# Performance work log

Hardware: AMD Instinct MI355X
Metric: run time of the kernel (lower is better)

Reference implementation:

```python
import jax, jax.numpy as jnp
import numpy as np
from jax.scipy.linalg import solve_triangular

B, L, HID, NH = 2, 1024, 1024, 4
DK = DV = 256
CONV_K, CHUNK, FIR_S_K, FIR_L_K = 4, 32, 3, 31
GATE_IN = HID + 3 * DV * 4 + DV * 4  # 5120
GATE_H = 2 * DV  # 512


def _l2norm(x):
    return x * jax.lax.rsqrt(jnp.sum(x * x, -1, keepdims=True) + 1e-6)


def _short_conv(x, w):
    # causal depthwise conv1d + silu. x: [b,l,c], w: [c,k]
    c, k = w.shape
    y = jax.lax.conv_general_dilated(x.transpose(0, 2, 1), w[:, None, :], (1,),
                                     [(k - 1, 0)], feature_group_count=c)
    return jax.nn.silu(y.transpose(0, 2, 1))


def _fir(x, f):
    # per-head depthwise causal FIR. x: [b,l,h,d], f: [h,d,k]
    b, l, h, d = x.shape
    k = f.shape[-1]
    xf = x.transpose(0, 2, 3, 1).reshape(b, h * d, l)
    y = jax.lax.conv_general_dilated(xf, f.reshape(h * d, 1, k), (1,),
                                     [(k - 1, 0)], feature_group_count=h * d)
    return y.reshape(b, h, d, l).transpose(0, 3, 1, 2)


def _delta_rule(q, k, v, beta, chunk=CHUNK):
    # q,k: [b,h,L,dk], v: [b,h,L,dv], beta: [b,h,L]; L % chunk == 0
    b, h, l, dk = q.shape
    dv = v.shape[-1]
    n = l // chunk
    q = _l2norm(q)
    k = _l2norm(k)
    v = v * beta[..., None]
    kb = k * beta[..., None]
    rs = lambda t: t.reshape(b, h, n, chunk, -1)
    q, k, v, kb = map(rs, (q, k, v, kb))
    # UT transform: serial forward substitution == unit-lower triangular solve
    A = -jnp.tril(jnp.einsum('bhncd,bhned->bhnce', kb, k), -1)  # strictly lower
    eye = jnp.eye(chunk, dtype=q.dtype)
    T = solve_triangular(eye - A, jnp.broadcast_to(eye, A.shape), lower=True)
    u = T @ v   # [b,h,n,c,dv]
    w = T @ kb  # [b,h,n,c,dk]
    mov = lambda t: jnp.moveaxis(t, 2, 0)

    def step(S, inp):
        qi, ki, ui, wi = inp  # [b,h,c,d]
        attn = jnp.tril(qi @ ki.transpose(0, 1, 3, 2))  # causal incl. diag
        u_i = ui - wi @ S
        o_i = qi @ S + attn @ u_i
        return S + ki.transpose(0, 1, 3, 2) @ u_i, o_i

    S0 = jnp.zeros((b, h, dk, dv), dtype=q.dtype)
    S, o = jax.lax.scan(step, S0, (mov(q), mov(k), mov(u), mov(w)))
    o = jnp.moveaxis(o, 0, 2).reshape(b, h, l, dv)
    return o, S


def _gate(hidden, branches, W1, b1, W2, b2, temp, eps_floor):
    def stats(p):
        m = p.mean(-1, keepdims=True)
        r = jnp.sqrt(jnp.clip((p * p).mean(-1, keepdims=True), 1e-8))
        mx = p.max(-1, keepdims=True)
        return jnp.concatenate([jnp.broadcast_to(m, p.shape),
                                jnp.broadcast_to(r, p.shape),
                                jnp.broadcast_to(mx, p.shape)], -1)

    b, l, h, d = branches[0].shape
    hb = jnp.broadcast_to(hidden[:, :, None, :], (b, l, h, hidden.shape[-1]))
    head_in = jnp.concatenate([hb] + [stats(p) for p in branches] + list(branches), -1)
    hmid = jax.nn.gelu(head_in @ W1 + b1, approximate=False)
    logits = hmid @ W2 + b2  # [b,l,h,4]
    t = jnp.clip(temp, 0.2, 10.0)[None, None, :, None]
    w = jax.nn.softmax(logits / t, -1)
    floor = jnp.clip(eps_floor, 1e-7, 0.1)[None, None]
    w = jnp.maximum(w, floor)
    return w / w.sum(-1, keepdims=True)


def setup_inputs() -> dict:
    key = jax.random.key(0)
    ks = jax.random.split(key, 16)
    s = 0.02
    inp = {
        'x': jax.random.normal(ks[0], (B, L, HID), jnp.float32),
        'Wq': jax.random.normal(ks[1], (HID, NH * DK), jnp.float32) * s,
        'Wk': jax.random.normal(ks[2], (HID, NH * DK), jnp.float32) * s,
        'Wv': jax.random.normal(ks[3], (HID, NH * DV), jnp.float32) * s,
        'Wb': jax.random.normal(ks[4], (HID, NH), jnp.float32) * s,
        'qc_w': jax.random.normal(ks[5], (NH * DK, CONV_K), jnp.float32) * 0.5,
        'kc_w': jax.random.normal(ks[6], (NH * DK, CONV_K), jnp.float32) * 0.5,
        'vc_w': jax.random.normal(ks[7], (NH * DV, CONV_K), jnp.float32) * 0.5,
        'gW1': jax.random.normal(ks[10], (GATE_IN, GATE_H), jnp.float32) * s,
        'gb1': jnp.zeros((GATE_H,), jnp.float32),
        'gW2': jax.random.normal(ks[11], (GATE_H, 4), jnp.float32) * s,
        'gb2': jnp.zeros((4,), jnp.float32),
        'temp': jnp.ones((NH,), jnp.float32),
        'eps_floor': jnp.full((NH, 4), 0.01, jnp.float32),
        'onorm_w': jnp.ones((DV,), jnp.float32),
        'Wo': jax.random.normal(ks[12], (NH * DV, HID), jnp.float32) * s,
    }
    # FIR filters: identity tap at last position + small noise (matches init intent)
    fs = jnp.zeros((NH, DV, FIR_S_K)).at[..., -1].set(1.0)
    fl = jnp.zeros((NH, DV, FIR_L_K)).at[..., -1].set(1.0)
    inp['fir_s'] = fs + s * jax.random.normal(ks[8], fs.shape, jnp.float32)
    inp['fir_l'] = fl + s * jax.random.normal(ks[9], fl.shape, jnp.float32)
    return inp


def reference(x, Wq, Wk, Wv, Wb, qc_w, kc_w, vc_w, fir_s, fir_l,
              gW1, gb1, gW2, gb2, temp, eps_floor, onorm_w, Wo):
    b, l, _ = x.shape
    q = _short_conv(x @ Wq, qc_w).reshape(b, l, NH, DK)
    k = _short_conv(x @ Wk, kc_w).reshape(b, l, NH, DK)
    v = _short_conv(x @ Wv, vc_w).reshape(b, l, NH, DV)
    beta = jax.nn.sigmoid(x @ Wb)  # [b,l,h]
    tr = lambda t: t.transpose(0, 2, 1, 3)
    delta_o, _ = _delta_rule(tr(q), tr(k), tr(v), beta.transpose(0, 2, 1))
    delta_o = tr(delta_o)  # [b,l,h,dv]
    branches = [_fir(v, fir_s), _fir(v, fir_l), delta_o, v]
    w = _gate(x, branches, gW1, gb1, gW2, gb2, temp, eps_floor)
    o = sum(w[..., i:i + 1] * branches[i] for i in range(4))
    o = o * jax.lax.rsqrt((o * o).mean(-1, keepdims=True) + 1e-5) * onorm_w
    return o.reshape(b, l, NH * DV) @ Wo
```

## Files before the change

kernel.cpp:

```cpp
#include <hip/hip_runtime.h>
#include <math.h>

#define BB 2
#define LL 1024
#define HIDD 1024
#define NH 4
#define DD 256
#define NCH 32
#define ROWS 2048
#define HROWS 8192

typedef long long i64;
typedef unsigned short u16t;
typedef unsigned int u32t;
typedef __attribute__((ext_vector_type(8))) short short8;
typedef __attribute__((ext_vector_type(4))) float f32x4;
#define MFMA_BF16(a, b, c) __builtin_amdgcn_mfma_f32_16x16x32_bf16(a, b, c, 0, 0, 0)

__device__ __forceinline__ float sigmoidf_(float x) { return 1.0f / (1.0f + expf(-x)); }

__device__ __forceinline__ u16t f2bf(float f) {
  u32t u = __float_as_uint(f);
  u = u + 0x7FFFu + ((u >> 16) & 1u);
  return (u16t)(u >> 16);
}
__device__ __forceinline__ u32t pk2(u16t a, u16t b) { return (u32t)a | ((u32t)b << 16); }

__device__ __forceinline__ u32t cvt_pk_bf16(float lo, float hi) {
  u32t r;
  asm("v_cvt_pk_bf16_f32 %0, %1, %2" : "=v"(r) : "v"(lo), "v"(hi));
  return r;
}

__device__ __forceinline__ void async_load16(const u16t* g, u16t* l) {
  __builtin_amdgcn_global_load_lds(
      (const __attribute__((address_space(1))) u32t*)g,
      (__attribute__((address_space(3))) u32t*)l, 16, 0, 0);
}

__device__ __forceinline__ void barrier_lds_only() {
  asm volatile("s_waitcnt lgkmcnt(0)" ::: "memory");
  __builtin_amdgcn_s_barrier();
  asm volatile("" ::: "memory");
}

template<int N>
__device__ __forceinline__ void block_reduce_sum(float* v, float* scratch) {
  int lane = threadIdx.x & 63, wid = threadIdx.x >> 6;
#pragma unroll
  for (int i = 0; i < N; i++) {
    float x = v[i];
#pragma unroll
    for (int off = 1; off < 64; off <<= 1) x += __shfl_xor(x, off);
    if (lane == 0) scratch[wid * N + i] = x;
  }
  __syncthreads();
#pragma unroll
  for (int i = 0; i < N; i++)
    v[i] = scratch[i] + scratch[N + i] + scratch[2 * N + i] + scratch[3 * N + i];
  __syncthreads();
}

__device__ __forceinline__ void transcast_body(
    const float* __restrict__ in, int ldin, u16t* __restrict__ out, int ldout,
    int nbi, int kbi, float (*tile)[33]) {
  int tx = threadIdx.x & 31, ty = threadIdx.x >> 5;
  int nb = nbi * 32, kb = kbi * 32;
#pragma unroll
  for (int r = 0; r < 4; r++)
    tile[ty + r * 8][tx] = in[(i64)(kb + ty + r * 8) * ldin + nb + tx];
  __syncthreads();
#pragma unroll
  for (int r = 0; r < 4; r++)
    out[(i64)(nb + ty + r * 8) * ldout + kb + tx] = f2bf(tile[tx][ty + r * 8]);
}

__global__ __launch_bounds__(256) void prep_kernel(
    const float* __restrict__ Wq, const float* __restrict__ Wk, const float* __restrict__ Wv,
    const float* __restrict__ x, const float* __restrict__ Wb,
    u16t* __restrict__ WqkvT, u16t* __restrict__ xbf, float* __restrict__ betab) {
  __shared__ float tile[32][33];
  int blk = blockIdx.x, t = threadIdx.x;
  if (blk < 3072) {
    int m = blk >> 10, bi = blk & 1023;
    const float* in = m == 0 ? Wq : m == 1 ? Wk : Wv;
    transcast_body(in, 1024, WqkvT + (i64)m * 1024 * 1024, 1024, bi & 31, bi >> 5, tile);
  } else if (blk < 5120) {
    i64 e = ((i64)(blk - 3072) * 256 + t) * 4;
    float4 v = *(const float4*)(x + e);
    uint2 o;
    o.x = pk2(f2bf(v.x), f2bf(v.y));
    o.y = pk2(f2bf(v.z), f2bf(v.w));
    *(uint2*)(xbf + e) = o;
  } else {
    int row = blk - 5120;
    float a[4] = {0, 0, 0, 0};
    for (int c = t; c < 1024; c += 256) {
      float xv = x[(i64)row * 1024 + c];
      float4 wv = *(const float4*)(Wb + c * 4);
      a[0] += xv * wv.x; a[1] += xv * wv.y; a[2] += xv * wv.z; a[3] += xv * wv.w;
    }
    block_reduce_sum<4>(a, (float*)tile);
    if (t == 0) {
#pragma unroll
      for (int g = 0; g < 4; g++) betab[row * 4 + g] = sigmoidf_(a[g]);
    }
  }
}

__device__ __forceinline__ void gemm_bt_body(
    const u16t* __restrict__ A, const u16t* __restrict__ B,
    float* __restrict__ C, int K, int ldc, int n0, int m0,
    u16t* As, u16t* Bs) {
  int t = threadIdx.x;
  int w = t >> 6, lane = t & 63;
  int l15 = lane & 15, quad = lane >> 4;
  int wm = (w & 1) * 64, wn = (w >> 1) * 64;
  f32x4 acc[4][4] = {};
  int c0 = 2 * w, c1 = 2 * w + 1;
  int srow0 = c0 * 16 + (lane >> 2);
  int srow1 = c1 * 16 + (lane >> 2);
  int scol = (lane & 3) * 8;
  const u16t* Ag0 = A + (i64)(m0 + srow0) * K + scol;
  const u16t* Ag1 = A + (i64)(m0 + srow1) * K + scol;
  const u16t* Bg0 = B + (i64)(n0 + srow0) * K + scol;
  const u16t* Bg1 = B + (i64)(n0 + srow1) * K + scol;
  int lb0 = c0 * 512, lb1 = c1 * 512;
  async_load16(Ag0, As + lb0);
  async_load16(Ag1, As + lb1);
  async_load16(Bg0, Bs + lb0);
  async_load16(Bg1, Bs + lb1);
  __syncthreads();
  int nt = K >> 5;
  for (int ti = 0; ti < nt; ++ti) {
    int cur = (ti & 1) << 12;
    if (ti + 1 < nt) {
      int nxt = ((ti + 1) & 1) << 12;
      int k = (ti + 1) << 5;
      async_load16(Ag0 + k, As + nxt + lb0);
      async_load16(Ag1 + k, As + nxt + lb1);
      async_load16(Bg0 + k, Bs + nxt + lb0);
      async_load16(Bg1 + k, Bs + nxt + lb1);
    }
    short8 a[4], b[4];
#pragma unroll
    for (int mt = 0; mt < 4; mt++)
      a[mt] = *(const short8*)&As[cur + (wm + mt * 16 + l15) * 32 + quad * 8];
#pragma unroll
    for (int ntt = 0; ntt < 4; ntt++)
      b[ntt] = *(const short8*)&Bs[cur + (wn + ntt * 16 + l15) * 32 + quad * 8];
#pragma unroll
    for (int mt = 0; mt < 4; mt++)
#pragma unroll
      for (int ntt = 0; ntt < 4; ntt++)
        acc[mt][ntt] = MFMA_BF16(a[mt], b[ntt], acc[mt][ntt]);
    __syncthreads();
  }
#pragma unroll
  for (int mt = 0; mt < 4; mt++) {
    int r0 = m0 + wm + mt * 16 + quad * 4;
#pragma unroll
    for (int nt2 = 0; nt2 < 4; nt2++) {
      int cc = n0 + wn + nt2 * 16 + l15;
#pragma unroll
      for (int rg = 0; rg < 4; rg++)
        C[(i64)(r0 + rg) * ldc + cc] = acc[mt][nt2][rg];
    }
  }
}

__global__ __launch_bounds__(256) void gemm_bt_kernel(
    const u16t* __restrict__ A, const u16t* __restrict__ B,
    float* __restrict__ C, int K, int ldc) {
  __shared__ u16t As[2 * 128 * 32];
  __shared__ u16t Bs[2 * 128 * 32];
  gemm_bt_body(A, B, C, K, ldc, blockIdx.x * 128, blockIdx.y * 128, As, Bs);
}

__global__ __launch_bounds__(256) void conv_silu3_kernel(
    const float* __restrict__ pre, const float* __restrict__ qw,
    const float* __restrict__ kw, const float* __restrict__ vw,
    float* __restrict__ qo, float* __restrict__ ko, float* __restrict__ vo,
    u16t* __restrict__ brcat) {
  int seg = blockIdx.x >> 11;
  int row = blockIdx.x & 2047;
  int l = row & 1023;
  int c = threadIdx.x * 4;
  const float* w = seg == 0 ? qw : seg == 1 ? kw : vw;
  float* out = seg == 0 ? qo : seg == 1 ? ko : vo;
  float4 w0 = *(const float4*)(w + (i64)(c + 0) * 4);
  float4 w1 = *(const float4*)(w + (i64)(c + 1) * 4);
  float4 w2 = *(const float4*)(w + (i64)(c + 2) * 4);
  float4 w3 = *(const float4*)(w + (i64)(c + 3) * 4);
  const float* base = pre + (i64)row * 3072 + (seg << 10) + c;
  float4 x0 = *(const float4*)(base);
  float4 acc;
  acc.x = w0.w * x0.x; acc.y = w1.w * x0.y; acc.z = w2.w * x0.z; acc.w = w3.w * x0.w;
  if (l >= 1) {
    float4 xm = *(const float4*)(base - 3072);
    acc.x += w0.z * xm.x; acc.y += w1.z * xm.y; acc.z += w2.z * xm.z; acc.w += w3.z * xm.w;
  }
  if (l >= 2) {
    float4 xm = *(const float4*)(base - 2 * 3072);
    acc.x += w0.y * xm.x; acc.y += w1.y * xm.y; acc.z += w2.y * xm.z; acc.w += w3.y * xm.w;
  }
  if (l >= 3) {
    float4 xm = *(const float4*)(base - 3 * 3072);
    acc.x += w0.x * xm.x; acc.y += w1.x * xm.y; acc.z += w2.x * xm.z; acc.w += w3.x * xm.w;
  }
  float4 r;
  r.x = acc.x * sigmoidf_(acc.x);
  r.y = acc.y * sigmoidf_(acc.y);
  r.z = acc.z * sigmoidf_(acc.z);
  r.w = acc.w * sigmoidf_(acc.w);
  *(float4*)(out + (i64)row * 1024 + c) = r;
  if (seg == 2) {
    uint2 o;
    o.x = cvt_pk_bf16(r.x, r.y);
    o.y = cvt_pk_bf16(r.z, r.w);
    *(uint2*)(brcat + ((i64)row * 4 + (c >> 8)) * 1024 + 768 + (c & 255)) = o;
  }
}

__global__ __launch_bounds__(256) void preprocess_kernel(
    const float* __restrict__ q, const float* __restrict__ k, const float* __restrict__ v,
    const float* __restrict__ beta, float* __restrict__ qn, float* __restrict__ kn,
    float* __restrict__ vb, float* __restrict__ kb, u16t* __restrict__ qnbf) {
  int t = threadIdx.x, lane = t & 63, wv = t >> 6;
  int row = blockIdx.x * 4 + wv;
  i64 base = (i64)row * 256 + lane * 4;
  float4 q4 = *(const float4*)(q + base);
  float4 k4 = *(const float4*)(k + base);
  float4 v4 = *(const float4*)(v + base);
  float s2[2];
  s2[0] = q4.x * q4.x + q4.y * q4.y + q4.z * q4.z + q4.w * q4.w;
  s2[1] = k4.x * k4.x + k4.y * k4.y + k4.z * k4.z + k4.w * k4.w;
#pragma unroll
  for (int off = 1; off < 64; off <<= 1) {
    s2[0] += __shfl_xor(s2[0], off);
    s2[1] += __shfl_xor(s2[1], off);
  }
  float qi = rsqrtf(s2[0] + 1e-6f), ki = rsqrtf(s2[1] + 1e-6f);
  float bet = beta[row];
  float4 qn4, kn4, vb4, kb4;
  qn4.x = q4.x * qi; qn4.y = q4.y * qi; qn4.z = q4.z * qi; qn4.w = q4.w * qi;
  kn4.x = k4.x * ki; kn4.y = k4.y * ki; kn4.z = k4.z * ki; kn4.w = k4.w * ki;
  vb4.x = v4.x * bet; vb4.y = v4.y * bet; vb4.z = v4.z * bet; vb4.w = v4.w * bet;
  kb4.x = kn4.x * bet; kb4.y = kn4.y * bet; kb4.z = kn4.z * bet; kb4.w = kn4.w * bet;
  *(float4*)(qn + base) = qn4;
  *(float4*)(kn + base) = kn4;
  *(float4*)(vb + base) = vb4;
  *(float4*)(kb + base) = kb4;
  int b = row >> 12, l = (row >> 2) & 1023, h = row & 3;
  uint2 o;
  o.x = cvt_pk_bf16(qn4.x, qn4.y);
  o.y = cvt_pk_bf16(qn4.z, qn4.w);
  *(uint2*)(qnbf + ((i64)(b * 4 + h) * 1024 + l) * 256 + lane * 4) = o;
}

__global__ __launch_bounds__(256) void phaseA2_kernel(
    const float* __restrict__ qn, const float* __restrict__ kn,
    const float* __restrict__ vb, const float* __restrict__ kb,
    float* __restrict__ u_g, u16t* __restrict__ w_bf, u16t* __restrict__ attn_bf,
    u16t* __restrict__ knT,
    const float* __restrict__ gW1, const float* __restrict__ Wo,
    u16t* __restrict__ W1hT, u16t* __restrict__ W1bT, u16t* __restrict__ WoT,
    float* __restrict__ wsum) {
  __shared__ __attribute__((aligned(16))) char smem[37376];
  int blk = blockIdx.x, t = threadIdx.x;
  if (blk < 256) {
    float (*KN)[260] = (float(*)[260])smem;
    float (*Ms)[32] = (float(*)[32])(smem + 33280);
    int i = blk & 31, bh = blk >> 5;
    int rbase = ((bh >> 2) * LL + i * 32) * NH + (bh & 3);
    i64 bhn = blk;
#pragma unroll
    for (int ii = 0; ii < 8; ii++) {
      int fid = t + ii * 256;
      int c = fid >> 6, dq = (fid & 63) << 2;
      *(float4*)&KN[c][dq] = *(const float4*)(kn + (i64)(rbase + c * NH) * 256 + dq);
    }
    __syncthreads();
    int c = t >> 3, e0 = (t & 7) * 4;
    const float* kbp = kb + (i64)(rbase + c * NH) * 256;
    const float* qp = qn + (i64)(rbase + c * NH) * 256;
    float am[4] = {0, 0, 0, 0}, aa[4] = {0, 0, 0, 0};
    for (int d = 0; d < 256; d += 4) {
      float4 kv = *(const float4*)(kbp + d);
      float4 qv = *(const float4*)(qp + d);
#pragma unroll
      for (int z = 0; z < 4; z++) {
        float4 nv = *(const float4*)&KN[e0 + z][d];
        am[z] += kv.x * nv.x + kv.y * nv.y + kv.z * nv.z + kv.w * nv.w;
        aa[z] += qv.x * nv.x + qv.y * nv.y + qv.z * nv.z + qv.w * nv.w;
      }
    }
    {
      uint2 o;
      u16t a0 = (e0 + 0 <= c) ? f2bf(aa[0]) : 0;
      u16t a1 = (e0 + 1 <= c) ? f2bf(aa[1]) : 0;
      u16t a2 = (e0 + 2 <= c) ? f2bf(aa[2]) : 0;
      u16t a3 = (e0 + 3 <= c) ? f2bf(aa[3]) : 0;
      o.x = pk2(a0, a1); o.y = pk2(a2, a3);
      *(uint2*)(attn_bf + bhn * 1024 + c * 32 + e0) = o;
    }
#pragma unroll
    for (int z = 0; z < 4; z++) {
      int e = e0 + z;
      Ms[c][e] = (e < c) ? am[z] : 0.0f;
    }
    __syncthreads();
    float uc[32], wc[32];
#pragma unroll
    for (int cc = 0; cc < 32; cc++) {
      float uval = vb[(i64)(rbase + cc * NH) * 256 + t];
      float wval = kb[(i64)(rbase + cc * NH) * 256 + t];
#pragma unroll
      for (int c2 = 0; c2 < cc; c2++) {
        float m = Ms[cc][c2];
        uval -= m * uc[c2];
        wval -= m * wc[c2];
      }
      uc[cc] = uval; wc[cc] = wval;
      u_g[(bhn * 32 + cc) * 256 + t] = uval;
      w_bf[(bhn * 32 + cc) * 256 + t] = f2bf(-wval);
    }
    int d = t;
    u16t o[32];
#pragma unroll
    for (int cc = 0; cc < 32; cc++) o[cc] = f2bf(KN[cc][d]);
#pragma unroll
    for (int z = 0; z < 4; z++) {
      uint4 vv;
      vv.x = pk2(o[z * 8 + 0], o[z * 8 + 1]);
      vv.y = pk2(o[z * 8 + 2], o[z * 8 + 3]);
      vv.z = pk2(o[z * 8 + 4], o[z * 8 + 5]);
      vv.w = pk2(o[z * 8 + 6], o[z * 8 + 7]);
      *(uint4*)(knT + (bhn * 256 + d) * 32 + z * 8) = vv;
    }
  } else if (blk < 2304) {
    float (*tile)[33] = (float(*)[33])smem;
    int pb = blk - 256;
    if (pb < 1024) {
      int which = pb >> 9, bi = pb & 511;
      const float* in = gW1 + (which ? (i64)4096 * 512 : 0);
      transcast_body(in, 512, which ? W1bT : W1hT, 1024, bi & 15, bi >> 4, tile);
    } else {
      int bi = pb - 1024;
      transcast_body(Wo, 1024, WoT, 1024, bi & 31, bi >> 5, tile);
    }
  } else {
    int bi = blk - 2304;
    int s12 = bi >> 1, col = (bi & 1) * 256 + t;
    const float* p = gW1 + (i64)(1024 + s12 * 256) * 512 + col;
    float acc = 0.0f;
    for (int r = 0; r < 256; r++) acc += p[(i64)r * 512];
    wsum[s12 * 512 + col] = acc;
  }
}

#define SROW 264
struct ScanBuf {
  short8 m8[8];
  f32x4 uc4;
  short8 af;
  short8 kf[4];
};

__device__ void delta_scan_body(
    int blk,
    const u16t* __restrict__ wbf, const u16t* __restrict__ knT,
    const float* __restrict__ u_g, const u16t* __restrict__ qnbf,
    const u16t* __restrict__ attnbf,
    float* __restrict__ dlt, u16t* __restrict__ brcat,
    u16t* Sbf, u16t* Ubf) {
  int t = threadIdx.x, w = t >> 6, lane = t & 63;
  int l15 = lane & 15, quad = lane >> 4;
  int bh = blk & 7, jb = blk >> 3, j0 = jb * 16;
  int b_ = bh >> 2, h_ = bh & 3;
  bool isU = (w < 2);
  int wc = isU ? w : (w - 2);
  for (int idx = t; idx < 16 * SROW; idx += 256) Sbf[idx] = 0;
  f32x4 accS[4] = {};
  __syncthreads();
  __builtin_amdgcn_s_setprio(1);

  auto load_chunk = [&](int i, ScanBuf& B) {
    i64 bhn = (i64)bh * 32 + i;
    const u16t* mbase = isU
        ? wbf + (bhn * 32 + wc * 16 + l15) * 256 + quad * 8
        : qnbf + ((i64)bh * 1024 + i * 32 + wc * 16 + l15) * 256 + quad * 8;
#pragma unroll
    for (int kd = 0; kd < 8; kd++) B.m8[kd] = *(const short8*)(mbase + kd * 32);
    if (isU) {
      int cm = wc * 16 + quad * 4;
#pragma unroll
      for (int r = 0; r < 4; r++)
        B.uc4[r] = u_g[(bhn * 32 + cm + r) * 256 + j0 + l15];
    } else {
      B.af = *(const short8*)(attnbf + bhn * 1024 + (wc * 16 + l15) * 32 + quad * 8);
    }
#pragma unroll
    for (int dt = 0; dt < 4; dt++)
      B.kf[dt] = *(const short8*)(knT + (bhn * 256 + w * 64 + dt * 16 + l15) * 32 + quad * 8);
  };

  auto process = [&](int i, ScanBuf& B) {
    f32x4 zero = {};
    f32x4 ca = isU ? B.uc4 : zero;
    f32x4 cb = zero;
#pragma unroll
    for (int kd = 0; kd < 4; kd++) {
      short8 sfa = *(const short8*)&Sbf[l15 * SROW + kd * 32 + quad * 8];
      short8 sfb = *(const short8*)&Sbf[l15 * SROW + (kd + 4) * 32 + quad * 8];
      ca = MFMA_BF16(B.m8[kd], sfa, ca);
      cb = MFMA_BF16(B.m8[kd + 4], sfb, cb);
    }
    f32x4 cacc;
#pragma unroll
    for (int r = 0; r < 4; r++) cacc[r] = ca[r] + cb[r];
    if (isU) {
      int cm = wc * 16 + quad * 4;
      uint2 o;
      o.x = cvt_pk_bf16(cacc[0], cacc[1]);
      o.y = cvt_pk_bf16(cacc[2], cacc[3]);
      *(uint2*)&Ubf[l15 * 40 + cm] = o;
    }
    barrier_lds_only();
    short8 bu = *(const short8*)&Ubf[l15 * 40 + quad * 8];
    if (!isU) {
      cacc = MFMA_BF16(B.af, bu, cacc);
#pragma unroll
      for (int rg = 0; rg < 4; rg++) {
        int l = i * 32 + wc * 16 + quad * 4 + rg;
        i64 row = ((i64)b_ * 1024 + l) * 4 + h_;
        dlt[row * 256 + j0 + l15] = cacc[rg];
        brcat[row * 1024 + 512 + j0 + l15] = f2bf(cacc[rg]);
      }
    }
#pragma unroll
    for (int dt = 0; dt < 4; dt++) accS[dt] = MFMA_BF16(B.kf[dt], bu, accS[dt]);
#pragma unroll
    for (int dt = 0; dt < 4; dt++) {
      uint2 o;
      o.x = cvt_pk_bf16(accS[dt][0], accS[dt][1]);
      o.y = cvt_pk_bf16(accS[dt][2], accS[dt][3]);
      *(uint2*)&Sbf[l15 * SROW + w * 64 + dt * 16 + quad * 4] = o;
    }
    barrier_lds_only();
  };

  ScanBuf b0, b1;
  load_chunk(0, b0);
#pragma unroll 1
  for (int ii = 0; ii < 16; ii++) {
    int i = ii * 2;
    load_chunk(i + 1, b1);
    process(i, b0);
    if (ii < 15) load_chunk(i + 2, b0);
    process(i + 1, b1);
  }
  __builtin_amdgcn_s_setprio(0);
}

__device__ void fir2_body(
    int blk, const float* __restrict__ v,
    const float* __restrict__ f_s, const float* __restrict__ f_l,
    float* __restrict__ fs, float* __restrict__ fl, u16t* __restrict__ brcat) {
  int t = threadIdx.x;
  int b = blk >> 8, h = (blk >> 6) & 3, lc = blk & 63;
  int l0 = lc * 16;
  float flw[31], fsw[3];
  const float* flp = f_l + ((i64)h * 256 + t) * 31;
#pragma unroll
  for (int j = 0; j < 31; j++) flw[j] = flp[j];
  const float* fsp = f_s + ((i64)h * 256 + t) * 3;
#pragma unroll
  for (int j = 0; j < 3; j++) fsw[j] = fsp[j];
  float win[46];
#pragma unroll
  for (int r = 0; r < 46; r++) {
    int l = l0 - 30 + r;
    win[r] = (l >= 0) ? v[(((i64)b * 1024 + l) * 4 + h) * 256 + t] : 0.0f;
  }
#pragma unroll
  for (int i = 0; i < 16; i++) {
    float al = 0.0f;
#pragma unroll
    for (int j = 0; j < 31; j++) al += flw[j] * win[i + j];
    float as = fsw[0] * win[i + 28] + fsw[1] * win[i + 29] + fsw[2] * win[i + 30];
    i64 row = ((i64)b * 1024 + (l0 + i)) * 4 + h;
    fs[row * 256 + t] = as;
    fl[row * 256 + t] = al;
    brcat[row * 1024 + t] = f2bf(as);
    brcat[row * 1024 + 256 + t] = f2bf(al);
  }
}

__global__ __launch_bounds__(256) void mega5_kernel(
    const u16t* __restrict__ wbf, const u16t* __restrict__ knT,
    const float* __restrict__ u_g, const u16t* __restrict__ qnbf,
    const u16t* __restrict__ attnbf, float* __restrict__ dlt, u16t* __restrict__ brcat,
    const float* __restrict__ vbuf, const float* __restrict__ firs,
    const float* __restrict__ firl, float* __restrict__ fs, float* __restrict__ fl,
    const u16t* __restrict__ xbf, const u16t* __restrict__ W1hT,
    float* __restrict__ hbase) {
  __shared__ __attribute__((aligned(16))) char smem[32768];
  int blk = blockIdx.x;
  if (blk < 128) {
    u16t* Sbf = (u16t*)smem;
    u16t* Ubf = Sbf + 16 * SROW;
    delta_scan_body(blk, wbf, knT, u_g, qnbf, attnbf, dlt, brcat, Sbf, Ubf);
  } else if (blk < 640) {
    fir2_body(blk - 128, vbuf, firs, firl, fs, fl, brcat);
  } else {
    int bi = blk - 640;
    u16t* As = (u16t*)smem;
    u16t* Bs = As + 2 * 128 * 32;
    gemm_bt_body(xbf, W1hT, hbase, 1024, 512, (bi & 3) * 128, (bi >> 2) * 128, As, Bs);
  }
}

__global__ __launch_bounds__(256) void gatemix_kernel(
    const float* __restrict__ hbase, const float* __restrict__ brW,
    const float* __restrict__ wsum,
    const float* __restrict__ gb1, const float* __restrict__ gW2,
    const float* __restrict__ gb2, const float* __restrict__ temp,
    const float* __restrict__ epsf,
    const float* __restrict__ fs, const float* __restrict__ fl,
    const float* __restrict__ dlt, const float* __restrict__ v,
    const float* __restrict__ onw, u16t* __restrict__ out) {
  int t = threadIdx.x, lane = t & 63, wv = t >> 6;
  int row = blockIdx.x * 4 + wv;
  int bl = row >> 2, h = row & 3;
  i64 base = (i64)row * 256 + lane * 4;
  float4 vfs = *(const float4*)(fs + base);
  float4 vfl = *(const float4*)(fl + base);
  float4 vdl = *(const float4*)(dlt + base);
  float4 vvv = *(const float4*)(v + base);
  float r8[8];
  r8[0] = vfs.x + vfs.y + vfs.z + vfs.w;
  r8[1] = vfs.x * vfs.x + vfs.y * vfs.y + vfs.z * vfs.z + vfs.w * vfs.w;
  r8[2] = vfl.x + vfl.y + vfl.z + vfl.w;
  r8[3] = vfl.x * vfl.x + vfl.y * vfl.y + vfl.z * vfl.z + vfl.w * vfl.w;
  r8[4] = vdl.x + vdl.y + vdl.z + vdl.w;
  r8[5] = vdl.x * vdl.x + vdl.y * vdl.y + vdl.z * vdl.z + vdl.w * vdl.w;
  r8[6] = vvv.x + vvv.y + vvv.z + vvv.w;
  r8[7] = vvv.x * vvv.x + vvv.y * vvv.y + vvv.z * vvv.z + vvv.w * vvv.w;
#pragma unroll
  for (int off = 1; off < 64; off <<= 1) {
#pragma unroll
    for (int i = 0; i < 8; i++) r8[i] += __shfl_xor(r8[i], off);
  }
  float m4[4];
  m4[0] = fmaxf(fmaxf(vfs.x, vfs.y), fmaxf(vfs.z, vfs.w));
  m4[1] = fmaxf(fmaxf(vfl.x, vfl.y), fmaxf(vfl.z, vfl.w));
  m4[2] = fmaxf(fmaxf(vdl.x, vdl.y), fmaxf(vdl.z, vdl.w));
  m4[3] = fmaxf(fmaxf(vvv.x, vvv.y), fmaxf(vvv.z, vvv.w));
#pragma unroll
  for (int off = 1; off < 64; off <<= 1) {
#pragma unroll
    for (int i = 0; i < 4; i++) m4[i] = fmaxf(m4[i], __shfl_xor(m4[i], off));
  }
  float st[12];
#pragma unroll
  for (int p = 0; p < 4; p++) {
    st[p * 3 + 0] = r8[p * 2] * (1.0f / 256.0f);
    st[p * 3 + 1] = sqrtf(fmaxf(r8[p * 2 + 1] * (1.0f / 256.0f), 1e-8f));
    st[p * 3 + 2] = m4[p];
  }
  float lg[4] = {0, 0, 0, 0};
#pragma unroll
  for (int jj = 0; jj < 8; jj++) {
    int o = jj * 64 + lane;
    float hm = hbase[(i64)bl * 512 + o] + brW[(i64)row * 512 + o] + gb1[o];
#pragma unroll
    for (int s = 0; s < 12; s++) hm += st[s] * wsum[s * 512 + o];
    float ge = 0.5f * hm * (1.0f + erff(hm * 0.70710678118654752f));
    float4 w2 = *(const float4*)(gW2 + o * 4);
    lg[0] += ge * w2.x; lg[1] += ge * w2.y; lg[2] += ge * w2.z; lg[3] += ge * w2.w;
  }
#pragma unroll
  for (int off = 1; off < 64; off <<= 1) {
#pragma unroll
    for (int i = 0; i < 4; i++) lg[i] += __shfl_xor(lg[i], off);
  }
  float tt = fminf(fmaxf(temp[h], 0.2f), 10.0f);
  float l0 = (lg[0] + gb2[0]) / tt;
  float l1 = (lg[1] + gb2[1]) / tt;
  float l2 = (lg[2] + gb2[2]) / tt;
  float l3 = (lg[3] + gb2[3]) / tt;
  float m = fmaxf(fmaxf(l0, l1), fmaxf(l2, l3));
  float e0 = expf(l0 - m), e1 = expf(l1 - m), e2 = expf(l2 - m), e3 = expf(l3 - m);
  float ssum = e0 + e1 + e2 + e3;
  float w0 = e0 / ssum, w1 = e1 / ssum, w2 = e2 / ssum, w3 = e3 / ssum;
  w0 = fmaxf(w0, fminf(fmaxf(epsf[h * 4 + 0], 1e-7f), 0.1f));
  w1 = fmaxf(w1, fminf(fmaxf(epsf[h * 4 + 1], 1e-7f), 0.1f));
  w2 = fmaxf(w2, fminf(fmaxf(epsf[h * 4 + 2], 1e-7f), 0.1f));
  w3 = fmaxf(w3, fminf(fmaxf(epsf[h * 4 + 3], 1e-7f), 0.1f));
  float s2 = w0 + w1 + w2 + w3;
  float g0 = w0 / s2, g1 = w1 / s2, g2 = w2 / s2, g3 = w3 / s2;
  float4 o4;
  o4.x = g0 * vfs.x + g1 * vfl.x + g2 * vdl.x + g3 * vvv.x;
  o4.y = g0 * vfs.y + g1 * vfl.y + g2 * vdl.y + g3 * vvv.y;
  o4.z = g0 * vfs.z + g1 * vfl.z + g2 * vdl.z + g3 * vvv.z;
  o4.w = g0 * vfs.w + g1 * vfl.w + g2 * vdl.w + g3 * vvv.w;
  float ss = o4.x * o4.x + o4.y * o4.y + o4.z * o4.z + o4.w * o4.w;
#pragma unroll
  for (int off = 1; off < 64; off <<= 1) ss += __shfl_xor(ss, off);
  float scale = rsqrtf(ss * (1.0f / 256.0f) + 1e-5f);
  float4 ow4 = *(const float4*)(onw + lane * 4);
  uint2 ow;
  ow.x = cvt_pk_bf16(o4.x * scale * ow4.x, o4.y * scale * ow4.y);
  ow.y = cvt_pk_bf16(o4.z * scale * ow4.z, o4.w * scale * ow4.w);
  *(uint2*)(out + (i64)bl * 1024 + h * 256 + lane * 4) = ow;
}

extern "C" void kernel_launch(void* const* d_in, const int* in_sizes, int n_in,
                              void* d_out, int out_size, void* d_ws, size_t ws_size,
                              hipStream_t stream) {
  (void)in_sizes; (void)n_in; (void)out_size; (void)ws_size;
  const float* x    = (const float*)d_in[0];
  const float* Wq   = (const float*)d_in[1];
  const float* Wk   = (const float*)d_in[2];
  const float* Wv   = (const float*)d_in[3];
  const float* Wb   = (const float*)d_in[4];
  const float* qcw  = (const float*)d_in[5];
  const float* kcw  = (const float*)d_in[6];
  const float* vcw  = (const float*)d_in[7];
  const float* gW1  = (const float*)d_in[8];
  const float* gb1  = (const float*)d_in[9];
  const float* gW2  = (const float*)d_in[10];
  const float* gb2  = (const float*)d_in[11];
  const float* temp = (const float*)d_in[12];
  const float* epsf = (const float*)d_in[13];
  const float* onw  = (const float*)d_in[14];
  const float* Wo   = (const float*)d_in[15];
  const float* firs = (const float*)d_in[16];
  const float* firl = (const float*)d_in[17];
  float* out = (float*)d_out;

  float* ws = (float*)d_ws;
  float* qkv_pre  = ws + 0;
  float* branchW  = ws + 0;
  float* hbase    = ws + 4194304;
  u16t*  W1hT     = (u16t*)(ws + 5242880);
  u16t*  W1bT     = (u16t*)(ws + 5505024);
  u16t*  WoT      = (u16t*)(ws + 5767168);
  u16t*  brcat    = (u16t*)(ws + 6291456);
  float* qbuf     = ws + 10485760; float* qn = qbuf;
  float* kbuf     = ws + 12582912; float* kn = kbuf;
  float* vbuf     = ws + 14680064;
  float* vb       = ws + 16777216;
  u16t*  omix_bf  = (u16t*)(ws + 16777216);
  float* kb       = ws + 18874368;
  float* dlt      = ws + 18874368;
  float* u_g      = ws + 20971520;
  u16t*  w_bf     = (u16t*)(ws + 23068672);
  u16t*  qn_bf    = (u16t*)(ws + 24117248);
  u16t*  knT      = (u16t*)(ws + 25165824);
  u16t*  attn_bf  = (u16t*)(ws + 26214400);
  float* fs       = ws + 26345472;
  float* fl       = ws + 28442624;
  u16t*  xbf      = (u16t*)(ws + 30539776);
  u16t*  WqkvT    = (u16t*)(ws + 31588352);
  float* betab    = ws + 33161216;
  float* wsum     = ws + 33267712;

  prep_kernel<<<7168, 256, 0, stream>>>(Wq, Wk, Wv, x, Wb, WqkvT, xbf, betab);
  gemm_bt_kernel<<<dim3(24, 16), 256, 0, stream>>>(xbf, WqkvT, qkv_pre, 1024, 3072);
  conv_silu3_kernel<<<6144, 256, 0, stream>>>(qkv_pre, qcw, kcw, vcw, qbuf, kbuf, vbuf, brcat);
  preprocess_kernel<<<2048, 256, 0, stream>>>(qbuf, kbuf, vbuf, betab, qn, kn, vb, kb, qn_bf);
  phaseA2_kernel<<<2328, 256, 0, stream>>>(qn, kn, vb, kb, u_g, w_bf, attn_bf, knT,
                                           gW1, Wo, W1hT, W1bT, WoT, wsum);
  mega5_kernel<<<704, 256, 0, stream>>>(w_bf, knT, u_g, qn_bf, attn_bf, dlt, brcat,
                                        vbuf, firs, firl, fs, fl,
                                        xbf, W1hT, hbase);
  gemm_bt_kernel<<<dim3(4, 64), 256, 0, stream>>>(brcat, W1bT, branchW, 1024, 512);
  gatemix_kernel<<<2048, 256, 0, stream>>>(hbase, branchW, wsum, gb1, gW2, gb2,
                                           temp, epsf, fs, fl, dlt, vbuf, onw, omix_bf);
  gemm_bt_kernel<<<dim3(8, 16), 256, 0, stream>>>(omix_bf, WoT, out, 1024, 1024);
}
```

Before: 316.6 us.

## Move FIR into phaseA kernel and overlap branch GEMM with delta scan

```diff
diff --git a/kernel.cpp b/kernel.cpp
--- a/kernel.cpp
+++ b/kernel.cpp
@@ -108,30 +108,29 @@
   }
 }
 
-__device__ __forceinline__ void gemm_bt_body(
+__device__ __forceinline__ void gemm_tiles_acc(
     const u16t* __restrict__ A, const u16t* __restrict__ B,
-    float* __restrict__ C, int K, int ldc, int n0, int m0,
-    u16t* As, u16t* Bs) {
+    i64 ld, int koff, int Kext, int n0, int m0,
+    u16t* As, u16t* Bs, f32x4 (&acc)[4][4]) {
   int t = threadIdx.x;
   int w = t >> 6, lane = t & 63;
   int l15 = lane & 15, quad = lane >> 4;
   int wm = (w & 1) * 64, wn = (w >> 1) * 64;
-  f32x4 acc[4][4] = {};
   int c0 = 2 * w, c1 = 2 * w + 1;
   int srow0 = c0 * 16 + (lane >> 2);
   int srow1 = c1 * 16 + (lane >> 2);
   int scol = (lane & 3) * 8;
-  const u16t* Ag0 = A + (i64)(m0 + srow0) * K + scol;
-  const u16t* Ag1 = A + (i64)(m0 + srow1) * K + scol;
-  const u16t* Bg0 = B + (i64)(n0 + srow0) * K + scol;
-  const u16t* Bg1 = B + (i64)(n0 + srow1) * K + scol;
+  const u16t* Ag0 = A + (i64)(m0 + srow0) * ld + koff + scol;
+  const u16t* Ag1 = A + (i64)(m0 + srow1) * ld + koff + scol;
+  const u16t* Bg0 = B + (i64)(n0 + srow0) * ld + koff + scol;
+  const u16t* Bg1 = B + (i64)(n0 + srow1) * ld + koff + scol;
   int lb0 = c0 * 512, lb1 = c1 * 512;
   async_load16(Ag0, As + lb0);
   async_load16(Ag1, As + lb1);
   async_load16(Bg0, Bs + lb0);
   async_load16(Bg1, Bs + lb1);
   __syncthreads();
-  int nt = K >> 5;
+  int nt = Kext >> 5;
   for (int ti = 0; ti < nt; ++ti) {
     int cur = (ti & 1) << 12;
     if (ti + 1 < nt) {
@@ -156,17 +155,36 @@
         acc[mt][ntt] = MFMA_BF16(a[mt], b[ntt], acc[mt][ntt]);
     __syncthreads();
   }
+}
+
+__device__ __forceinline__ void gemm_store(
+    float* __restrict__ C, int ldc, int n0, int m0, f32x4 (&acc)[4][4], bool add) {
+  int t = threadIdx.x;
+  int w = t >> 6, lane = t & 63;
+  int l15 = lane & 15, quad = lane >> 4;
+  int wm = (w & 1) * 64, wn = (w >> 1) * 64;
 #pragma unroll
   for (int mt = 0; mt < 4; mt++) {
     int r0 = m0 + wm + mt * 16 + quad * 4;
 #pragma unroll
-    for (int nt2 = 0; nt2 < 4; nt2++) {
-      int cc = n0 + wn + nt2 * 16 + l15;
-#pragma unroll
-      for (int rg = 0; rg < 4; rg++)
-        C[(i64)(r0 + rg) * ldc + cc] = acc[mt][nt2][rg];
-    }
-  }
+    for (int nt = 0; nt < 4; nt++) {
+      int cc = n0 + wn + nt * 16 + l15;
+#pragma unroll
+      for (int rg = 0; rg < 4; rg++) {
+        i64 idx = (i64)(r0 + rg) * ldc + cc;
+        C[idx] = add ? (C[idx] + acc[mt][nt][rg]) : acc[mt][nt][rg];
+      }
+    }
+  }
+}
+
+__device__ __forceinline__ void gemm_bt_body(
+    const u16t* __restrict__ A, const u16t* __restrict__ B,
+    float* __restrict__ C, int K, int ldc, int n0, int m0,
+    u16t* As, u16t* Bs) {
+  f32x4 acc[4][4] = {};
+  gemm_tiles_acc(A, B, K, 0, K, n0, m0, As, Bs, acc);
+  gemm_store(C, ldc, n0, m0, acc, false);
 }
 
 __global__ __launch_bounds__(256) void gemm_bt_kernel(
@@ -258,14 +276,51 @@
   *(uint2*)(qnbf + ((i64)(b * 4 + h) * 1024 + l) * 256 + lane * 4) = o;
 }
 
-__global__ __launch_bounds__(256) void phaseA2_kernel(
+__device__ void fir2_body(
+    int blk, const float* __restrict__ v,
+    const float* __restrict__ f_s, const float* __restrict__ f_l,
+    float* __restrict__ fs, float* __restrict__ fl, u16t* __restrict__ brcat) {
+  int t = threadIdx.x;
+  int b = blk >> 8, h = (blk >> 6) & 3, lc = blk & 63;
+  int l0 = lc * 16;
+  float flw[31], fsw[3];
+  const float* flp = f_l + ((i64)h * 256 + t) * 31;
+#pragma unroll
+  for (int j = 0; j < 31; j++) flw[j] = flp[j];
+  const float* fsp = f_s + ((i64)h * 256 + t) * 3;
+#pragma unroll
+  for (int j = 0; j < 3; j++) fsw[j] = fsp[j];
+  float win[46];
+#pragma unroll
+  for (int r = 0; r < 46; r++) {
+    int l = l0 - 30 + r;
+    win[r] = (l >= 0) ? v[(((i64)b * 1024 + l) * 4 + h) * 256 + t] : 0.0f;
+  }
+#pragma unroll
+  for (int i = 0; i < 16; i++) {
+    float al = 0.0f;
+#pragma unroll
+    for (int j = 0; j < 31; j++) al += flw[j] * win[i + j];
+    float as = fsw[0] * win[i + 28] + fsw[1] * win[i + 29] + fsw[2] * win[i + 30];
+    i64 row = ((i64)b * 1024 + (l0 + i)) * 4 + h;
+    fs[row * 256 + t] = as;
+    fl[row * 256 + t] = al;
+    brcat[row * 1024 + t] = f2bf(as);
+    brcat[row * 1024 + 256 + t] = f2bf(al);
+  }
+}
+
+__global__ __launch_bounds__(256) void phaseA3_kernel(
     const float* __restrict__ qn, const float* __restrict__ kn,
     const float* __restrict__ vb, const float* __restrict__ kb,
     float* __restrict__ u_g, u16t* __restrict__ w_bf, u16t* __restrict__ attn_bf,
     u16t* __restrict__ knT,
     const float* __restrict__ gW1, const float* __restrict__ Wo,
     u16t* __restrict__ W1hT, u16t* __restrict__ W1bT, u16t* __restrict__ WoT,
-    float* __restrict__ wsum) {
+    float* __restrict__ wsum,
+    const float* __restrict__ vbuf, const float* __restrict__ firs,
+    const float* __restrict__ firl, float* __restrict__ fs, float* __restrict__ fl,
+    u16t* __restrict__ brcat) {
   __shared__ __attribute__((aligned(16))) char smem[37376];
   int blk = blockIdx.x, t = threadIdx.x;
   if (blk < 256) {
@@ -349,13 +404,15 @@
       int bi = pb - 1024;
       transcast_body(Wo, 1024, WoT, 1024, bi & 31, bi >> 5, tile);
     }
-  } else {
+  } else if (blk < 2328) {
     int bi = blk - 2304;
     int s12 = bi >> 1, col = (bi & 1) * 256 + t;
     const float* p = gW1 + (i64)(1024 + s12 * 256) * 512 + col;
     float acc = 0.0f;
     for (int r = 0; r < 256; r++) acc += p[(i64)r * 512];
     wsum[s12 * 512 + col] = acc;
+  } else {
+    fir2_body(blk - 2328, vbuf, firs, firl, fs, fl, brcat);
   }
 }
 
@@ -463,62 +520,46 @@
   __builtin_amdgcn_s_setprio(0);
 }
 
-__device__ void fir2_body(
-    int blk, const float* __restrict__ v,
-    const float* __restrict__ f_s, const float* __restrict__ f_l,
-    float* __restrict__ fs, float* __restrict__ fl, u16t* __restrict__ brcat) {
-  int t = threadIdx.x;
-  int b = blk >> 8, h = (blk >> 6) & 3, lc = blk & 63;
-  int l0 = lc * 16;
-  float flw[31], fsw[3];
-  const float* flp = f_l + ((i64)h * 256 + t) * 31;
-#pragma unroll
-  for (int j = 0; j < 31; j++) flw[j] = flp[j];
-  const float* fsp = f_s + ((i64)h * 256 + t) * 3;
-#pragma unroll
-  for (int j = 0; j < 3; j++) fsw[j] = fsp[j];
-  float win[46];
-#pragma unroll
-  for (int r = 0; r < 46; r++) {
-    int l = l0 - 30 + r;
-    win[r] = (l >= 0) ? v[(((i64)b * 1024 + l) * 4 + h) * 256 + t] : 0.0f;
-  }
-#pragma unroll
-  for (int i = 0; i < 16; i++) {
-    float al = 0.0f;
-#pragma unroll
-    for (int j = 0; j < 31; j++) al += flw[j] * win[i + j];
-    float as = fsw[0] * win[i + 28] + fsw[1] * win[i + 29] + fsw[2] * win[i + 30];
-    i64 row = ((i64)b * 1024 + (l0 + i)) * 4 + h;
-    fs[row * 256 + t] = as;
-    fl[row * 256 + t] = al;
-    brcat[row * 1024 + t] = f2bf(as);
-    brcat[row * 1024 + 256 + t] = f2bf(al);
-  }
-}
-
-__global__ __launch_bounds__(256) void mega5_kernel(
+__global__ __launch_bounds__(256) void mega6_kernel(
     const u16t* __restrict__ wbf, const u16t* __restrict__ knT,
     const float* __restrict__ u_g, const u16t* __restrict__ qnbf,
     const u16t* __restrict__ attnbf, float* __restrict__ dlt, u16t* __restrict__ brcat,
-    const float* __restrict__ vbuf, const float* __restrict__ firs,
-    const float* __restrict__ firl, float* __restrict__ fs, float* __restrict__ fl,
     const u16t* __restrict__ xbf, const u16t* __restrict__ W1hT,
-    float* __restrict__ hbase) {
+    float* __restrict__ hbase,
+    const u16t* __restrict__ W1bT, float* __restrict__ branchW) {
   __shared__ __attribute__((aligned(16))) char smem[32768];
   int blk = blockIdx.x;
   if (blk < 128) {
     u16t* Sbf = (u16t*)smem;
     u16t* Ubf = Sbf + 16 * SROW;
     delta_scan_body(blk, wbf, knT, u_g, qnbf, attnbf, dlt, brcat, Sbf, Ubf);
-  } else if (blk < 640) {
-    fir2_body(blk - 128, vbuf, firs, firl, fs, fl, brcat);
-  } else {
-    int bi = blk - 640;
+  } else if (blk < 192) {
+    int bi = blk - 128;
     u16t* As = (u16t*)smem;
     u16t* Bs = As + 2 * 128 * 32;
     gemm_bt_body(xbf, W1hT, hbase, 1024, 512, (bi & 3) * 128, (bi >> 2) * 128, As, Bs);
-  }
+  } else {
+    int bi = blk - 192;
+    u16t* As = (u16t*)smem;
+    u16t* Bs = As + 2 * 128 * 32;
+    int n0 = (bi & 3) * 128, m0 = (bi >> 2) * 128;
+    f32x4 acc[4][4] = {};
+    gemm_tiles_acc(brcat, W1bT, 1024, 768, 256, n0, m0, As, Bs, acc);
+    gemm_tiles_acc(brcat, W1bT, 1024, 0, 512, n0, m0, As, Bs, acc);
+    gemm_store(branchW, 512, n0, m0, acc, false);
+  }
+}
+
+__global__ __launch_bounds__(256) void branchw_dlt_kernel(
+    const u16t* __restrict__ brcat, const u16t* __restrict__ W1bT,
+    float* __restrict__ branchW) {
+  __shared__ u16t As[2 * 128 * 32];
+  __shared__ u16t Bs[2 * 128 * 32];
+  int bi = blockIdx.x;
+  int n0 = (bi & 3) * 128, m0 = (bi >> 2) * 128;
+  f32x4 acc[4][4] = {};
+  gemm_tiles_acc(brcat, W1bT, 1024, 512, 256, n0, m0, As, Bs, acc);
+  gemm_store(branchW, 512, n0, m0, acc, true);
 }
 
 __global__ __launch_bounds__(256) void gatemix_kernel(
@@ -671,12 +712,12 @@
   gemm_bt_kernel<<<dim3(24, 16), 256, 0, stream>>>(xbf, WqkvT, qkv_pre, 1024, 3072);
   conv_silu3_kernel<<<6144, 256, 0, stream>>>(qkv_pre, qcw, kcw, vcw, qbuf, kbuf, vbuf, brcat);
   preprocess_kernel<<<2048, 256, 0, stream>>>(qbuf, kbuf, vbuf, betab, qn, kn, vb, kb, qn_bf);
-  phaseA2_kernel<<<2328, 256, 0, stream>>>(qn, kn, vb, kb, u_g, w_bf, attn_bf, knT,
-                                           gW1, Wo, W1hT, W1bT, WoT, wsum);
-  mega5_kernel<<<704, 256, 0, stream>>>(w_bf, knT, u_g, qn_bf, attn_bf, dlt, brcat,
-                                        vbuf, firs, firl, fs, fl,
-                                        xbf, W1hT, hbase);
-  gemm_bt_kernel<<<dim3(4, 64), 256, 0, stream>>>(brcat, W1bT, branchW, 1024, 512);
+  phaseA3_kernel<<<2840, 256, 0, stream>>>(qn, kn, vb, kb, u_g, w_bf, attn_bf, knT,
+                                           gW1, Wo, W1hT, W1bT, WoT, wsum,
+                                           vbuf, firs, firl, fs, fl, brcat);
+  mega6_kernel<<<448, 256, 0, stream>>>(w_bf, knT, u_g, qn_bf, attn_bf, dlt, brcat,
+                                        xbf, W1hT, hbase, W1bT, branchW);
+  branchw_dlt_kernel<<<256, 256, 0, stream>>>(brcat, W1bT, branchW);
   gatemix_kernel<<<2048, 256, 0, stream>>>(hbase, branchW, wsum, gb1, gW2, gb2,
                                            temp, epsf, fs, fl, dlt, vbuf, onw, omix_bf);
   gemm_bt_kernel<<<dim3(8, 16), 256, 0, stream>>>(omix_bf, WoT, out, 1024, 1024);
```

Measured after the change: 313.9 us. Within noise of the previous version (-0.8%).
